# Kernel tuning notes

Hardware: AMD Instinct MI355X
Metric: run time of the kernel (lower is better)

Reference implementation:

```python
import jax, jax.numpy as jnp
import numpy as np

N_EMBD = 1024
N_HEAD = 16
HEAD_DIM = N_EMBD // N_HEAD
D_FF = 4 * N_EMBD


def dyt(x, alpha, gamma, beta):
    # Dynamic Tanh normalizer: gamma * tanh(alpha * x) + beta
    return gamma * jnp.tanh(x * alpha) + beta


def setup_inputs() -> dict:
    key = jax.random.key(0)
    ks = jax.random.split(key, 9)
    C, F = N_EMBD, D_FF
    s = 0.02
    return {
        "x": jax.random.normal(ks[0], (2, 2048, C), dtype=jnp.float32),
        "alpha": jnp.ones((1,), jnp.float32) * 0.5,
        "gamma": jnp.ones((C,), jnp.float32),
        "beta": jnp.zeros((C,), jnp.float32),
        "w_attn": jax.random.normal(ks[1], (C, 3 * C), jnp.float32) * s,
        "b_attn": jnp.zeros((3 * C,), jnp.float32),
        "w_proj": jax.random.normal(ks[2], (C, C), jnp.float32) * s,
        "b_proj": jnp.zeros((C,), jnp.float32),
        "w_fc": jax.random.normal(ks[3], (C, F), jnp.float32) * s,
        "b_fc": jnp.zeros((F,), jnp.float32),
        "w_fc2": jax.random.normal(ks[4], (F, C), jnp.float32) * s,
        "b_fc2": jnp.zeros((C,), jnp.float32),
    }


def reference(x, alpha, gamma, beta, w_attn, b_attn, w_proj, b_proj,
              w_fc, b_fc, w_fc2, b_fc2):
    B, T, C = x.shape
    H, D = N_HEAD, HEAD_DIM

    # --- attention branch (pre-norm with DyT) ---
    h = dyt(x, alpha, gamma, beta)
    qkv = h @ w_attn + b_attn                      # [B,T,3C]
    q, k, v = jnp.split(qkv, 3, axis=-1)
    q = q.reshape(B, T, H, D).transpose(0, 2, 1, 3)  # [B,H,T,D]
    k = k.reshape(B, T, H, D).transpose(0, 2, 1, 3)
    v = v.reshape(B, T, H, D).transpose(0, 2, 1, 3)

    scores = jnp.einsum('bhqd,bhkd->bhqk', q, k) / jnp.sqrt(jnp.asarray(D, x.dtype))
    causal = jnp.tril(jnp.ones((T, T), bool))
    scores = jnp.where(causal[None, None], scores, -jnp.inf)
    attn = jax.nn.softmax(scores, axis=-1)          # [B,H,T,T]
    out = jnp.einsum('bhqk,bhkd->bhqd', attn, v)    # [B,H,T,D]
    out = out.transpose(0, 2, 1, 3).reshape(B, T, C)
    x = x + (out @ w_proj + b_proj)

    # --- MLP branch (pre-norm with same DyT params, as in source) ---
    h2 = dyt(x, alpha, gamma, beta)
    mlp = jax.nn.gelu(h2 @ w_fc + b_fc, approximate=False) @ w_fc2 + b_fc2
    return x + mlp
```

## Files before the change

kernel.cpp:

```cpp
#include <hip/hip_runtime.h>
#include <cstdint>
#include <cstddef>

typedef __bf16 bf16;
typedef __bf16 bf16x8 __attribute__((ext_vector_type(8)));
typedef __bf16 bf16x4 __attribute__((ext_vector_type(4)));
typedef float f32x4 __attribute__((ext_vector_type(4)));

#define DEVI __device__ __forceinline__

DEVI void gload_lds16(const bf16* g, bf16* l) {
    __builtin_amdgcn_global_load_lds(
        (const __attribute__((address_space(1))) void*)(const void*)g,
        (__attribute__((address_space(3))) void*)(void*)l, 16, 0, 0);
}

__global__ void conv_t_kernel(const float* __restrict__ W, bf16* __restrict__ Wt,
                              int K, int N) {
    __shared__ float tile[64][65];
    const int tid = threadIdx.x;
    const int c  = tid & 63;
    const int r4 = tid >> 6;
    const int n0 = blockIdx.x * 64;
    const int k0 = blockIdx.y * 64;
#pragma unroll
    for (int r = 0; r < 64; r += 4)
        tile[r + r4][c] = W[(size_t)(k0 + r + r4) * N + n0 + c];
    __syncthreads();
#pragma unroll
    for (int r = 0; r < 64; r += 4)
        Wt[(size_t)(n0 + r + r4) * K + k0 + c] = (bf16)tile[c][r + r4];
}

__global__ void dyt_kernel(const float* __restrict__ x, const float* __restrict__ alpha,
                           const float* __restrict__ gamma, const float* __restrict__ beta,
                           bf16* __restrict__ h, int total) {
    int i4 = (blockIdx.x * 256 + threadIdx.x) * 4;
    if (i4 >= total) return;
    float a = alpha[0];
    float4 xv = *(const float4*)&x[i4];
    int c = i4 & 1023;
    float4 g  = *(const float4*)&gamma[c];
    float4 bt = *(const float4*)&beta[c];
    bf16x4 o;
    o[0] = (bf16)(g.x * tanhf(xv.x * a) + bt.x);
    o[1] = (bf16)(g.y * tanhf(xv.y * a) + bt.y);
    o[2] = (bf16)(g.z * tanhf(xv.z * a) + bt.z);
    o[3] = (bf16)(g.w * tanhf(xv.w * a) + bt.w);
    *(bf16x4*)&h[i4] = o;
}

__global__ void reduce2_kernel(const float* __restrict__ p, const float* __restrict__ bias,
                               const float* __restrict__ resid, float* __restrict__ out,
                               int total) {
    int i4 = (blockIdx.x * 256 + threadIdx.x) * 4;
    if (i4 >= total) return;
    float4 a = *(const float4*)&p[i4];
    float4 bsec = *(const float4*)&p[(size_t)total + i4];
    float4 r = *(const float4*)&resid[i4];
    int c = i4 & 1023;
    float4 bb = *(const float4*)&bias[c];
    float4 o;
    o.x = a.x + bsec.x + r.x + bb.x;
    o.y = a.y + bsec.y + r.y + bb.y;
    o.z = a.z + bsec.z + r.z + bb.z;
    o.w = a.w + bsec.w + r.w + bb.w;
    *(float4*)&out[i4] = o;
}

__global__ void reduce2_dyt_kernel(const float* __restrict__ p, const float* __restrict__ bias,
                                   const float* __restrict__ resid,
                                   float* __restrict__ xout, bf16* __restrict__ hout,
                                   const float* __restrict__ alpha,
                                   const float* __restrict__ gamma,
                                   const float* __restrict__ beta, int total) {
    int i4 = (blockIdx.x * 256 + threadIdx.x) * 4;
    if (i4 >= total) return;
    float a = alpha[0];
    float4 p0 = *(const float4*)&p[i4];
    float4 p1 = *(const float4*)&p[(size_t)total + i4];
    float4 r  = *(const float4*)&resid[i4];
    int c = i4 & 1023;
    float4 bb = *(const float4*)&bias[c];
    float4 g  = *(const float4*)&gamma[c];
    float4 bt = *(const float4*)&beta[c];
    float4 v;
    v.x = p0.x + p1.x + r.x + bb.x;
    v.y = p0.y + p1.y + r.y + bb.y;
    v.z = p0.z + p1.z + r.z + bb.z;
    v.w = p0.w + p1.w + r.w + bb.w;
    *(float4*)&xout[i4] = v;
    bf16x4 o;
    o[0] = (bf16)(g.x * tanhf(v.x * a) + bt.x);
    o[1] = (bf16)(g.y * tanhf(v.y * a) + bt.y);
    o[2] = (bf16)(g.z * tanhf(v.z * a) + bt.z);
    o[3] = (bf16)(g.w * tanhf(v.w * a) + bt.w);
    *(bf16x4*)&hout[i4] = o;
}

template<int OP>
__global__ void gemm_kernel(const bf16* __restrict__ A, const bf16* __restrict__ Wt,
                            const float* __restrict__ bias, const float* resid,
                            float* outf, bf16* outb,
                            const float* __restrict__ alpha_p,
                            const float* __restrict__ gamma,
                            const float* __restrict__ beta,
                            int M, int N, int K, int lda, int ldb) {
    __shared__ bf16 As[2][128 * 32];
    __shared__ bf16 Bs[2][128 * 32];
    const int tid  = threadIdx.x;
    const int lane = tid & 63;
    const int w    = tid >> 6;
    const int wr   = w >> 1, wc = w & 1;

    const int nwgx = gridDim.x;
    const int nwg  = gridDim.x * gridDim.y;
    const int orig = blockIdx.y * nwgx + blockIdx.x;
    const int cpx  = nwg >> 3;
    const int swz  = (orig & 7) * cpx + (orig >> 3);
    const int bm = (swz / nwgx) * 128;
    const int bn = (swz % nwgx) * 128;
    const int kz = blockIdx.z * K;

    f32x4 acc[4][4] = {};

    const int srow = tid >> 2;
    const int sgrp = ((tid & 3) ^ ((srow >> 1) & 3)) * 8;
    const bf16* a0 = A  + (size_t)(bm + srow) * lda + kz + sgrp;
    const bf16* a1 = a0 + (size_t)64 * lda;
    const bf16* b0 = Wt + (size_t)(bn + srow) * ldb + kz + sgrp;
    const bf16* b1 = b0 + (size_t)64 * ldb;

    auto stage = [&](int buf) {
        gload_lds16(a0, &As[buf][tid * 8]);
        gload_lds16(a1, &As[buf][2048 + tid * 8]);
        gload_lds16(b0, &Bs[buf][tid * 8]);
        gload_lds16(b1, &Bs[buf][2048 + tid * 8]);
        a0 += 32; a1 += 32; b0 += 32; b1 += 32;
    };

    const int lh = lane >> 4, lm = lane & 15;
    const int arow = wr * 64 + lm;
    const int brow = wc * 64 + lm;
    const int gsw = (lh ^ ((lm >> 1) & 3)) * 8;

    stage(0);
    __syncthreads();

    const int nk = K >> 5;
    for (int kt = 0; kt < nk; ++kt) {
        const int cur = kt & 1;
        if (kt + 1 < nk) stage(cur ^ 1);
        bf16x8 af[4], bfr[4];
#pragma unroll
        for (int i = 0; i < 4; i++)
            af[i] = *(const bf16x8*)&As[cur][(arow + i * 16) * 32 + gsw];
#pragma unroll
        for (int i = 0; i < 4; i++)
            bfr[i] = *(const bf16x8*)&Bs[cur][(brow + i * 16) * 32 + gsw];
#pragma unroll
        for (int i = 0; i < 4; i++)
#pragma unroll
            for (int j = 0; j < 4; j++)
                acc[i][j] = __builtin_amdgcn_mfma_f32_16x16x32_bf16(af[i], bfr[j], acc[i][j], 0, 0, 0);
        __syncthreads();
    }

#pragma unroll
    for (int i = 0; i < 4; i++) {
        const int row0 = bm + wr * 64 + i * 16 + lh * 4;
#pragma unroll
        for (int jf = 0; jf < 4; jf++) {
            const int col = bn + wc * 64 + jf * 16 + lm;
            const float bval = (OP == 4) ? 0.f : bias[col];
#pragma unroll
            for (int r = 0; r < 4; r++) {
                const int row = row0 + r;
                const size_t idx = (size_t)row * N + col;
                float v = acc[i][jf][r] + bval;
                if (OP == 0) {
                    const float qs = (col < 1024) ? 0.18033688011f : 1.0f;
                    outb[idx] = (bf16)(v * qs);
                } else if (OP == 1) {
                    v += resid[idx];
                    outf[idx] = v;
                    float hh = gamma[col] * tanhf(v * alpha_p[0]) + beta[col];
                    outb[idx] = (bf16)hh;
                } else if (OP == 2) {
                    float g = 0.5f * v * (1.0f + erff(v * 0.70710678118f));
                    outb[idx] = (bf16)g;
                } else if (OP == 3) {
                    v += resid[idx];
                    outf[idx] = v;
                } else {
                    outf[(size_t)blockIdx.z * M * N + idx] = v;
                }
            }
        }
    }
}

__global__ void attn_kernel(const bf16* __restrict__ qkv, bf16* __restrict__ out) {
    const int j  = blockIdx.x;
    const int bh = blockIdx.y;
    const int b = bh >> 4, h = bh & 15;
    const int tid = threadIdx.x, lane = tid & 63, w = tid >> 6;
    const int T = 2048;
    const size_t C3 = 3072;
    const bf16* qb = qkv + (size_t)b * T * C3 + h * 64;
    const bf16* kb = qb + 1024;
    const bf16* vb = qb + 2048;

    __shared__ bf16 Ks[2][64][64];
    __shared__ bf16 Vt[2][64][72];
    __shared__ bf16 Pl[4][16][72];

    const int tA = j, tB = 31 - j;
    const int qA = tA * 64 + w * 16;
    const int qB = tB * 64 + w * 16;
    const int lm = lane & 15;
    const int lh = lane >> 4;

    bf16x8 qfA0, qfA1, qfB0, qfB1;
    {
        size_t qo = (size_t)(qA + lm) * C3 + lh * 8;
        qfA0 = *(const bf16x8*)&qb[qo];
        qfA1 = *(const bf16x8*)&qb[qo + 32];
        qo = (size_t)(qB + lm) * C3 + lh * 8;
        qfB0 = *(const bf16x8*)&qb[qo];
        qfB1 = *(const bf16x8*)&qb[qo + 32];
    }
    f32x4 accA[4] = {}, accB[4] = {};
    float mA = -1e30f, lA = 0.f, mB = -1e30f, lB = 0.f;

    const int nt = tB + 1;
    const int sg = tid & 7;
    const int sq = tid >> 3;
    bf16x8 rv[4];

    const int krow = tid >> 3;
    const int kcb  = tid & 7;
    const int kcbs = (kcb ^ (krow & 7)) * 8;
    auto stageK = [&](int buf, int k0) {
        gload_lds16(&kb[(size_t)(k0 + krow) * C3 + kcbs],      &Ks[buf][0][0]  + tid * 8);
        gload_lds16(&kb[(size_t)(k0 + 32 + krow) * C3 + kcbs], &Ks[buf][32][0] + tid * 8);
    };
    auto loadV = [&](int k0) {
        if (tid < 128) {
#pragma unroll
            for (int i = 0; i < 4; ++i)
                rv[i] = *(const bf16x8*)&vb[(size_t)(k0 + sq * 4 + i) * C3 + sg * 8];
        }
    };
    auto writeV = [&](int buf) {
        if (tid < 128) {
            const int cbase = ((((sq >> 1) ^ sg) & 7) << 3) + ((sq & 1) << 2);
#pragma unroll
            for (int e = 0; e < 8; ++e) {
                bf16x4 wv;
                wv[0] = rv[0][e]; wv[1] = rv[1][e]; wv[2] = rv[2][e]; wv[3] = rv[3][e];
                *(bf16x4*)&Vt[buf][sg * 8 + e][cbase] = wv;
            }
        }
    };

    auto pass = [&](const bf16x8& q0, const bf16x8& q1, f32x4 (&acc)[4],
                    float& mS, float& lS, int qg, bool diag, int buf, int k0) {
        f32x4 s[4];
#pragma unroll
        for (int f = 0; f < 4; ++f) {
            const int row = f * 16 + lm;
            const int sw = (row & 7);
            bf16x8 kf0v = *(const bf16x8*)&Ks[buf][row][(lh ^ sw) * 8];
            bf16x8 kf1v = *(const bf16x8*)&Ks[buf][row][((lh + 4) ^ sw) * 8];
            f32x4 z = {};
            z = __builtin_amdgcn_mfma_f32_16x16x32_bf16(kf0v, q0, z, 0, 0, 0);
            z = __builtin_amdgcn_mfma_f32_16x16x32_bf16(kf1v, q1, z, 0, 0, 0);
            s[f] = z;
        }
        if (diag) {
#pragma unroll
            for (int f = 0; f < 4; ++f)
#pragma unroll
                for (int r = 0; r < 4; ++r) {
                    const int kgl = k0 + f * 16 + lh * 4 + r;
                    s[f][r] = (kgl > qg) ? -1e30f : s[f][r];
                }
        }
        float a0 = fmaxf(fmaxf(s[0][0], s[0][1]), s[0][2]);
        float a1 = fmaxf(fmaxf(s[0][3], s[1][0]), s[1][1]);
        float a2 = fmaxf(fmaxf(s[1][2], s[1][3]), s[2][0]);
        float a3 = fmaxf(fmaxf(s[2][1], s[2][2]), s[2][3]);
        float a4 = fmaxf(fmaxf(s[3][0], s[3][1]), s[3][2]);
        float b0 = fmaxf(fmaxf(a0, a1), a2);
        float b1 = fmaxf(fmaxf(a3, a4), s[3][3]);
        float pm = fmaxf(b0, b1);
        pm = fmaxf(pm, __shfl_xor(pm, 16));
        pm = fmaxf(pm, __shfl_xor(pm, 32));
        if (!__all(pm - mS <= 8.f)) {
            const float mnew = fmaxf(mS, pm);
            const float corr = __builtin_amdgcn_exp2f(mS - mnew);
            mS = mnew;
            lS *= corr;
#pragma unroll
            for (int df = 0; df < 4; ++df)
#pragma unroll
                for (int r = 0; r < 4; ++r) acc[df][r] *= corr;
        }
        float rs = 0.f;
#pragma unroll
        for (int f = 0; f < 4; ++f) {
            bf16x4 pw;
#pragma unroll
            for (int r = 0; r < 4; ++r) {
                const float pv = __builtin_amdgcn_exp2f(s[f][r] - mS);
                rs += pv;
                pw[r] = (bf16)pv;
            }
            *(bf16x4*)&Pl[w][lm][f * 16 + lh * 4] = pw;
        }
        rs += __shfl_xor(rs, 16);
        rs += __shfl_xor(rs, 32);
        lS += rs;
#pragma unroll
        for (int kk = 0; kk < 2; ++kk) {
            bf16x8 pa = *(const bf16x8*)&Pl[w][lm][kk * 32 + lh * 8];
            const int kblk = 4 * kk + lh;
#pragma unroll
            for (int df = 0; df < 4; ++df) {
                const int dr = df * 16 + lm;
                bf16x8 vf = *(const bf16x8*)&Vt[buf][dr][((kblk ^ ((dr >> 3) & 7)) << 3)];
                acc[df] = __builtin_amdgcn_mfma_f32_16x16x32_bf16(vf, pa, acc[df], 0, 0, 0);
            }
        }
    };

    stageK(0, 0);
    loadV(0);
    writeV(0);
    __syncthreads();

    for (int kt = 0; kt < nt; ++kt) {
        const int k0 = kt * 64;
        const int buf = kt & 1;
        if (kt + 1 < nt) {
            stageK(buf ^ 1, k0 + 64);
            loadV(k0 + 64);
        }
        if (kt <= tA)
            pass(qfA0, qfA1, accA, mA, lA, qA + lm, kt == tA, buf, k0);
        if (kt + 1 < nt) writeV(buf ^ 1);
        pass(qfB0, qfB1, accB, mB, lB, qB + lm, kt == tB, buf, k0);
        __syncthreads();
    }

    bf16* obase = out + (size_t)b * T * 1024 + h * 64;
    {
        const float linv = 1.0f / lA;
        bf16* ob = obase + (size_t)(qA + lm) * 1024;
#pragma unroll
        for (int df = 0; df < 4; ++df) {
            bf16x4 st;
#pragma unroll
            for (int r = 0; r < 4; ++r) st[r] = (bf16)(accA[df][r] * linv);
            *(bf16x4*)&ob[df * 16 + lh * 4] = st;
        }
    }
    {
        const float linv = 1.0f / lB;
        bf16* ob = obase + (size_t)(qB + lm) * 1024;
#pragma unroll
        for (int df = 0; df < 4; ++df) {
            bf16x4 st;
#pragma unroll
            for (int r = 0; r < 4; ++r) st[r] = (bf16)(accB[df][r] * linv);
            *(bf16x4*)&ob[df * 16 + lh * 4] = st;
        }
    }
}

extern "C" void kernel_launch(void* const* d_in, const int* in_sizes, int n_in,
                              void* d_out, int out_size, void* d_ws, size_t ws_size,
                              hipStream_t stream) {
    const float* x      = (const float*)d_in[0];
    const float* alpha  = (const float*)d_in[1];
    const float* gamma  = (const float*)d_in[2];
    const float* beta   = (const float*)d_in[3];
    const float* w_attn = (const float*)d_in[4];
    const float* b_attn = (const float*)d_in[5];
    const float* w_proj = (const float*)d_in[6];
    const float* b_proj = (const float*)d_in[7];
    const float* w_fc   = (const float*)d_in[8];
    const float* b_fc   = (const float*)d_in[9];
    const float* w_fc2  = (const float*)d_in[10];
    const float* b_fc2  = (const float*)d_in[11];
    float* out = (float*)d_out;

    const int M = 4096, C = 1024, F = 4096;
    char* ws = (char*)d_ws;
    bf16* wt_attn = (bf16*)ws;
    bf16* wt_proj = wt_attn + (size_t)3 * C * C;
    bf16* wt_fc   = wt_proj + (size_t)C * C;
    bf16* wt_fc2  = wt_fc   + (size_t)F * C;
    bf16* hbuf    = wt_fc2  + (size_t)C * F;
    bf16* qkvbuf  = hbuf    + (size_t)M * C;
    bf16* aout    = qkvbuf  + (size_t)M * F;
    float* x2     = (float*)(aout + (size_t)M * C);
    float* part   = x2 + (size_t)M * C;
    const size_t need = (size_t)(88 + 32) * 1024 * 1024;
    const bool splitK = ws_size >= need;

    dim3 blk(256);
    conv_t_kernel<<<dim3(3 * C / 64, C / 64), blk, 0, stream>>>(w_attn, wt_attn, C, 3 * C);
    conv_t_kernel<<<dim3(C / 64, C / 64),     blk, 0, stream>>>(w_proj, wt_proj, C, C);
    conv_t_kernel<<<dim3(F / 64, C / 64),     blk, 0, stream>>>(w_fc,   wt_fc,   C, F);
    conv_t_kernel<<<dim3(C / 64, F / 64),     blk, 0, stream>>>(w_fc2,  wt_fc2,  F, C);

    dyt_kernel<<<dim3(M * C / 1024), blk, 0, stream>>>(x, alpha, gamma, beta, hbuf, M * C);

    gemm_kernel<0><<<dim3(3 * C / 128, M / 128), blk, 0, stream>>>(
        hbuf, wt_attn, b_attn, nullptr, nullptr, qkvbuf, nullptr, nullptr, nullptr,
        M, 3 * C, C, C, C);

    attn_kernel<<<dim3(16, 32), blk, 0, stream>>>(qkvbuf, aout);

    if (splitK) {
        gemm_kernel<4><<<dim3(C / 128, M / 128, 2), blk, 0, stream>>>(
            aout, wt_proj, b_proj, nullptr, part, nullptr, nullptr, nullptr, nullptr,
            M, C, C / 2, C, C);
        reduce2_dyt_kernel<<<dim3(M * C / 1024), blk, 0, stream>>>(
            part, b_proj, x, x2, hbuf, alpha, gamma, beta, M * C);
    } else {
        gemm_kernel<1><<<dim3(C / 128, M / 128), blk, 0, stream>>>(
            aout, wt_proj, b_proj, x, x2, hbuf, alpha, gamma, beta,
            M, C, C, C, C);
    }

    gemm_kernel<2><<<dim3(F / 128, M / 128), blk, 0, stream>>>(
        hbuf, wt_fc, b_fc, nullptr, nullptr, qkvbuf, nullptr, nullptr, nullptr,
        M, F, C, C, C);

    if (splitK) {
        gemm_kernel<4><<<dim3(C / 128, M / 128, 2), blk, 0, stream>>>(
            qkvbuf, wt_fc2, b_fc2, nullptr, part, nullptr, nullptr, nullptr, nullptr,
            M, C, F / 2, F, F);
        reduce2_kernel<<<dim3(M * C / 1024), blk, 0, stream>>>(part, b_fc2, x2, out, M * C);
    } else {
        gemm_kernel<3><<<dim3(C / 128, M / 128), blk, 0, stream>>>(
            qkvbuf, wt_fc2, b_fc2, x2, out, nullptr, nullptr, nullptr, nullptr,
            M, C, F, F, F);
    }
}
```

Before: 252.7 us.

## Use fast tanh/GELU approximations, shrink attention LDS padding, add MFMA priority

Replaces the library tanhf in the DyT kernels and the GEMM epilogue with an exp2/rcp-based tanh. Swaps the exact erf GELU for the sigmoid form of the tanh-approximate GELU, which is cheaper in the FC epilogue but deviates slightly from the exact reference. Reduces the padding of the attention kernel's V-transpose and P tiles from 72 to 68 columns. Also raises wave priority around the MFMA sections with s_setprio. The 68-column stride makes rows 136 bytes wide, so the 16-byte vector LDS reads are no longer 16-byte aligned and may be split or may conflict.

```diff
diff --git a/kernel.cpp b/kernel.cpp
--- a/kernel.cpp
+++ b/kernel.cpp
@@ -13,6 +13,11 @@
     __builtin_amdgcn_global_load_lds(
         (const __attribute__((address_space(1))) void*)(const void*)g,
         (__attribute__((address_space(3))) void*)(void*)l, 16, 0, 0);
+}
+
+DEVI float fast_tanh(float y) {
+    float t = __builtin_amdgcn_exp2f(2.88539008f * y);
+    return 1.f - 2.f * __builtin_amdgcn_rcpf(1.f + t);
 }
 
 __global__ void conv_t_kernel(const float* __restrict__ W, bf16* __restrict__ Wt,
@@ -43,10 +48,10 @@
     float4 g  = *(const float4*)&gamma[c];
     float4 bt = *(const float4*)&beta[c];
     bf16x4 o;
-    o[0] = (bf16)(g.x * tanhf(xv.x * a) + bt.x);
-    o[1] = (bf16)(g.y * tanhf(xv.y * a) + bt.y);
-    o[2] = (bf16)(g.z * tanhf(xv.z * a) + bt.z);
-    o[3] = (bf16)(g.w * tanhf(xv.w * a) + bt.w);
+    o[0] = (bf16)(g.x * fast_tanh(xv.x * a) + bt.x);
+    o[1] = (bf16)(g.y * fast_tanh(xv.y * a) + bt.y);
+    o[2] = (bf16)(g.z * fast_tanh(xv.z * a) + bt.z);
+    o[3] = (bf16)(g.w * fast_tanh(xv.w * a) + bt.w);
     *(bf16x4*)&h[i4] = o;
 }
 
@@ -91,10 +96,10 @@
     v.w = p0.w + p1.w + r.w + bb.w;
     *(float4*)&xout[i4] = v;
     bf16x4 o;
-    o[0] = (bf16)(g.x * tanhf(v.x * a) + bt.x);
-    o[1] = (bf16)(g.y * tanhf(v.y * a) + bt.y);
-    o[2] = (bf16)(g.z * tanhf(v.z * a) + bt.z);
-    o[3] = (bf16)(g.w * tanhf(v.w * a) + bt.w);
+    o[0] = (bf16)(g.x * fast_tanh(v.x * a) + bt.x);
+    o[1] = (bf16)(g.y * fast_tanh(v.y * a) + bt.y);
+    o[2] = (bf16)(g.z * fast_tanh(v.z * a) + bt.z);
+    o[3] = (bf16)(g.w * fast_tanh(v.w * a) + bt.w);
     *(bf16x4*)&hout[i4] = o;
 }
 
@@ -184,10 +189,12 @@
                 } else if (OP == 1) {
                     v += resid[idx];
                     outf[idx] = v;
-                    float hh = gamma[col] * tanhf(v * alpha_p[0]) + beta[col];
+                    float hh = gamma[col] * fast_tanh(v * alpha_p[0]) + beta[col];
                     outb[idx] = (bf16)hh;
                 } else if (OP == 2) {
-                    float g = 0.5f * v * (1.0f + erff(v * 0.70710678118f));
+                    float xc = v * (1.f + 0.044715f * v * v);
+                    float g = v * __builtin_amdgcn_rcpf(
+                        1.f + __builtin_amdgcn_exp2f(-2.30220795f * xc));
                     outb[idx] = (bf16)g;
                 } else if (OP == 3) {
                     v += resid[idx];
@@ -212,8 +219,8 @@
     const bf16* vb = qb + 2048;
 
     __shared__ bf16 Ks[2][64][64];
-    __shared__ bf16 Vt[2][64][72];
-    __shared__ bf16 Pl[4][16][72];
+    __shared__ bf16 Vt[2][64][68];
+    __shared__ bf16 Pl[4][16][68];
 
     const int tA = j, tB = 31 - j;
     const int qA = tA * 64 + w * 16;
@@ -267,6 +274,7 @@
     auto pass = [&](const bf16x8& q0, const bf16x8& q1, f32x4 (&acc)[4],
                     float& mS, float& lS, int qg, bool diag, int buf, int k0) {
         f32x4 s[4];
+        __builtin_amdgcn_s_setprio(1);
 #pragma unroll
         for (int f = 0; f < 4; ++f) {
             const int row = f * 16 + lm;
@@ -278,6 +286,7 @@
             z = __builtin_amdgcn_mfma_f32_16x16x32_bf16(kf1v, q1, z, 0, 0, 0);
             s[f] = z;
         }
+        __builtin_amdgcn_s_setprio(0);
         if (diag) {
 #pragma unroll
             for (int f = 0; f < 4; ++f)
@@ -322,6 +331,7 @@
         rs += __shfl_xor(rs, 16);
         rs += __shfl_xor(rs, 32);
         lS += rs;
+        __builtin_amdgcn_s_setprio(1);
 #pragma unroll
         for (int kk = 0; kk < 2; ++kk) {
             bf16x8 pa = *(const bf16x8*)&Pl[w][lm][kk * 32 + lh * 8];
@@ -333,6 +343,7 @@
                 acc[df] = __builtin_amdgcn_mfma_f32_16x16x32_bf16(vf, pa, acc[df], 0, 0, 0);
             }
         }
+        __builtin_amdgcn_s_setprio(0);
     };
 
     stageK(0, 0);
```

New measurement: 247.7 us. 1.02x faster.
